# Kernel optimization log

Measured on AMD Instinct MI355X. Metric: run time of the kernel, lower is better.

## Reference

```python
import jax, jax.numpy as jnp
import numpy as np

H = 1024
F = 1024


def _lstm_cell(x, h, c, Wih, Whh, b):
    # PyTorch gate order: i, f, g, o
    gates = x @ Wih.T + h @ Whh.T + b
    i, f, g, o = jnp.split(gates, 4, axis=-1)
    c = jax.nn.sigmoid(f) * c + jax.nn.sigmoid(i) * jnp.tanh(g)
    h = jax.nn.sigmoid(o) * jnp.tanh(c)
    return h, c


def setup_inputs() -> dict:
    key = jax.random.key(0)
    ks = iter(jax.random.split(key, 32))
    def rn(shape, s=0.05):
        return (s * jax.random.normal(next(ks), shape)).astype(jnp.float32)
    return {
        "tsn_feat_seq": rn((4096, F), 1.0),
        "W_fe": rn((H, F)), "b_fe": rn((H,)),
        "gW_ih0": rn((4 * H, 2 * H)), "gW_ihR": rn((4, 4 * H, H)),
        "gW_hh": rn((5, 4 * H, H)), "gb_ih": rn((5, 4 * H)), "gb_hh": rn((5, 4 * H)),
        "rW_ih": rn((4 * H, 2 * H)), "rW_hh": rn((4 * H, H)),
        "rb_ih": rn((4 * H,)), "rb_hh": rn((4 * H,)),
        "Wp": rn((H, 3 * H)), "bp": rn((H,)),
        "We2a": rn((2513, H)), "be2a": rn((2513,)),
        "We2v": rn((125, H)), "be2v": rn((125,)),
        "We2n": rn((352, H)), "be2n": rn((352,)),
    }


def reference(tsn_feat_seq, W_fe, b_fe, gW_ih0, gW_ihR, gW_hh, gb_ih, gb_hh,
              rW_ih, rW_hh, rb_ih, rb_hh, Wp, bp,
              We2a, be2a, We2v, be2v, We2n, be2n):
    # feat embedding of max-pooled TSN features (batch is always 1 after max)
    fs = jnp.max(tsn_feat_seq, axis=0) @ W_fe.T + b_fe          # [H]
    cur_action = (fs @ We2a.T + be2a)[None, :]                   # [1, 2513]

    # 5-layer goal LSTM, single time step, zero initial states;
    # input = concat(feat_state, zero action_state)
    z = jnp.zeros(H, fs.dtype)
    x = jnp.concatenate([fs, z])                                 # [2H]
    h, _ = _lstm_cell(x, z, z, gW_ih0, gW_hh[0], gb_ih[0] + gb_hh[0])
    for k in range(4):
        h, _ = _lstm_cell(h, z, z, gW_ihR[k], gW_hh[k + 1], gb_ih[k + 1] + gb_hh[k + 1])
    g = h                                                        # goal_state [H]

    rb = rb_ih + rb_hh

    def expand(a_in, f_in, best_d, best_f):
        # 10 single-layer LSTM steps with FIXED input (as in the source loop)
        xin = jnp.concatenate([a_in, f_in])                      # [2H]
        def rnn_step(carry, _):
            hh, cc = carry
            hh, cc = _lstm_cell(xin, hh, cc, rW_ih, rW_hh, rb)
            return (hh, cc), hh
        _, a_js = jax.lax.scan(rnn_step, (z, z), None, length=10)   # [10, H]
        # featpredictor: relu(Linear(concat(feat, action, goal))); dropout = eval identity
        pf = jnp.concatenate([jnp.broadcast_to(f_in, (10, H)), a_js,
                              jnp.broadcast_to(g, (10, H))], axis=1)  # [10, 3H]
        nfs = jax.nn.relu(pf @ Wp.T + bp)                        # [10, H]
        # sequential greedy best-feat update defines the scores (order matters)
        def score_step(carry, nf):
            bd, bf = carry
            d = jnp.sum((nf - g) ** 2) / H
            s = bd - d
            upd = d < bd
            return (jnp.where(upd, d, bd), jnp.where(upd, nf, bf)), s
        (bd, bf), scores = jax.lax.scan(score_step, (best_d, best_f), nfs)
        return a_js, nfs, scores, bd, bf

    # expansion 1: root node (action=0, feat=fs); best_feat_state starts at fs
    bd0 = jnp.sum((fs - g) ** 2) / H
    a1, f1, s1, bd1, bf1 = expand(z, fs, bd0, fs)
    # priority queue pops lowest score -> expansion 2 from that node
    i_star = jnp.argmin(s1)
    a2in = a1[i_star]
    f2in = f1[i_star]
    a2, f2, s2, _, _ = expand(a2in, f2in, bd1, bf1)

    # chain means: exp1 chain = [root, child]; exp2 chain = [root, n2, child]
    am = jnp.concatenate([a1 / 2.0, (a2in + a2) / 3.0], axis=0)        # [20, H]
    fm = jnp.concatenate([(fs + f1) / 2.0, (fs + f2in + f2) / 3.0], axis=0)
    scores = jnp.concatenate([s1.at[i_star].set(jnp.inf), s2])          # popped node removed
    _, idx = jax.lax.top_k(-scores, 2)                                  # 2 lowest scores, ascending
    pa = am[idx]                                                        # [2, H]
    pfeat = fm[idx]                                                     # [2, H]
    pgoal = jnp.broadcast_to(g, (2, H))

    pred_actions = pa @ We2a.T + be2a                                   # [2, 2513]
    pred_verbs = pa @ We2v.T + be2v                                     # [2, 125]
    pred_nouns = pa @ We2n.T + be2n                                     # [2, 352]
    # returned feat_state is the feat of the last popped (expanded) node
    return (pred_actions, pred_verbs, pred_nouns, pfeat, pgoal, f2in[None, :], cur_action)
```

## Files before the change

kernel.cpp:

```cpp
#include <hip/hip_runtime.h>
#include <math.h>


__device__ __forceinline__ float sigf(float x) { return 1.0f / (1.0f + expf(-x)); }

__device__ __forceinline__ float wave_red(float v) {
#pragma unroll
    for (int s = 32; s; s >>= 1) v += __shfl_down(v, s, 64);
    return v;
}

__device__ __forceinline__ float dotf(const float* __restrict__ w,
                                      const float* __restrict__ x, int lane) {
    float acc = 0.f;
#pragma unroll
    for (int j = 0; j < 4; ++j) {
        float4 a = *reinterpret_cast<const float4*>(w + j * 256 + lane * 4);
        float4 b = *reinterpret_cast<const float4*>(x + j * 256 + lane * 4);
        acc += a.x * b.x + a.y * b.y + a.z * b.z + a.w * b.w;
    }
    return acc;
}

__global__ void colmax_part_k(const float* __restrict__ tsn, float* __restrict__ part) {
    int tid = threadIdx.x;
    const float4* t4 = reinterpret_cast<const float4*>(tsn);
    float4 m = make_float4(-INFINITY, -INFINITY, -INFINITY, -INFINITY);
    int r0 = blockIdx.x * 512;
    for (int r = r0; r < r0 + 512; ++r) {
        float4 v = t4[(size_t)r * 256 + tid];
        m.x = fmaxf(m.x, v.x); m.y = fmaxf(m.y, v.y);
        m.z = fmaxf(m.z, v.z); m.w = fmaxf(m.w, v.w);
    }
    reinterpret_cast<float4*>(part + (size_t)blockIdx.x * 1024)[tid] = m;
}
__global__ void colmax_fin_k(const float* __restrict__ part, float* __restrict__ maxv) {
    int c = blockIdx.x * 256 + threadIdx.x;
    float m = -INFINITY;
    for (int b = 0; b < 8; ++b) m = fmaxf(m, part[b * 1024 + c]);
    maxv[c] = m;
}

__global__ void gemv_k(const float* __restrict__ W, int ld, int nrows,
                       const float* __restrict__ xA, int offA,
                       const float* __restrict__ xB, int offB,
                       const float* __restrict__ b1,
                       const float* __restrict__ b2,
                       float* __restrict__ yF, float* __restrict__ yOut) {
    int wave = threadIdx.x >> 6, lane = threadIdx.x & 63;
    int row = blockIdx.x * 4 + wave;
    if (row >= nrows) return;
    const float* wr = W + (size_t)row * ld;
    float acc = 0.f;
    if (xA) acc += dotf(wr + offA, xA, lane);
    if (xB) acc += dotf(wr + offB, xB, lane);
    acc = wave_red(acc);
    if (lane == 0) {
        if (b1) acc += b1[row];
        if (b2) acc += b2[row];
        if (yF) yF[row] = acc;
        if (yOut) yOut[row] = acc;
    }
}

__global__ void lstm_fused_k(const float* __restrict__ W, int ld, int off,
                             const float* __restrict__ x,
                             const float* __restrict__ b1,
                             const float* __restrict__ b2,
                             const float* __restrict__ gx,
                             const float* __restrict__ cc_in,
                             float* __restrict__ cc_out,
                             float* __restrict__ h_out) {
    __shared__ float glds[4][4];
    int wave = threadIdx.x >> 6, lane = threadIdx.x & 63;
    int j0 = blockIdx.x * 4;
#pragma unroll
    for (int jj = 0; jj < 4; ++jj) {
        int row = wave * 1024 + j0 + jj;
        float acc = dotf(W + (size_t)row * ld + off, x, lane);
        acc = wave_red(acc);
        if (lane == 0) {
            if (b1) acc += b1[row];
            if (b2) acc += b2[row];
            if (gx) acc += gx[row];
            glds[wave][jj] = acc;
        }
    }
    __syncthreads();
    if (threadIdx.x < 4) {
        int jj = threadIdx.x, j = j0 + jj;
        float gi = glds[0][jj], gf = glds[1][jj], gg = glds[2][jj], go = glds[3][jj];
        float c = sigf(gi) * tanhf(gg);
        if (cc_in) c += sigf(gf) * cc_in[j];
        float h = sigf(go) * tanhf(c);
        if (cc_out) cc_out[j] = c;
        h_out[j] = h;
    }
}

__global__ void cell0_k(const float* __restrict__ gx, float* __restrict__ cc_out,
                        float* __restrict__ h_out) {
    int j = blockIdx.x * 256 + threadIdx.x;
    float gi = gx[j], gg = gx[2048 + j], go = gx[3072 + j];
    float c = sigf(gi) * tanhf(gg);
    float h = sigf(go) * tanhf(c);
    cc_out[j] = c;
    h_out[j] = h;
}

__global__ void nfs_k(const float* __restrict__ Wp, const float* __restrict__ ajs,
                      const float* __restrict__ sv, float* __restrict__ nfs) {
    int wave = threadIdx.x >> 6, lane = threadIdx.x & 63;
    int i = blockIdx.x * 4 + wave;
    const float* wr = Wp + (size_t)i * 3072 + 1024;
    float wf[16];
#pragma unroll
    for (int j = 0; j < 4; ++j) {
        float4 a = *reinterpret_cast<const float4*>(wr + j * 256 + lane * 4);
        wf[j * 4 + 0] = a.x; wf[j * 4 + 1] = a.y; wf[j * 4 + 2] = a.z; wf[j * 4 + 3] = a.w;
    }
    float acc[10];
#pragma unroll
    for (int t = 0; t < 10; ++t) acc[t] = 0.f;
#pragma unroll
    for (int t = 0; t < 10; ++t) {
        const float* a = ajs + t * 1024;
#pragma unroll
        for (int j = 0; j < 4; ++j) {
            float4 b = *reinterpret_cast<const float4*>(a + j * 256 + lane * 4);
            acc[t] += wf[j * 4 + 0] * b.x + wf[j * 4 + 1] * b.y +
                      wf[j * 4 + 2] * b.z + wf[j * 4 + 3] * b.w;
        }
    }
#pragma unroll
    for (int t = 0; t < 10; ++t) {
        float r = wave_red(acc[t]);
        if (lane == 0) nfs[t * 1024 + i] = fmaxf(sv[i] + r, 0.f);
    }
}

__global__ void scores1_k(const float* __restrict__ nfs1, const float* __restrict__ g,
                          const float* __restrict__ fs, const float* __restrict__ ajs1,
                          float* __restrict__ s1, float* __restrict__ bd1_out,
                          int* __restrict__ istar_out, float* __restrict__ a2in,
                          float* __restrict__ f2in, float* __restrict__ out_f2in) {
    __shared__ float red[256];
    __shared__ float d[11];
    __shared__ int istar_sh;
    int tid = threadIdx.x;
    for (int t = 0; t < 11; ++t) {
        const float* v = (t < 10) ? (nfs1 + t * 1024) : fs;
        float p = 0.f;
        for (int j = tid * 4; j < tid * 4 + 4; ++j) { float df = v[j] - g[j]; p += df * df; }
        red[tid] = p; __syncthreads();
        for (int s = 128; s; s >>= 1) { if (tid < s) red[tid] += red[tid + s]; __syncthreads(); }
        if (tid == 0) d[t] = red[0] * (1.0f / 1024.0f);
        __syncthreads();
    }
    if (tid == 0) {
        float bd = d[10];
        float smin = INFINITY; int im = 0;
        for (int t = 0; t < 10; ++t) {
            float s = bd - d[t];
            s1[t] = s;
            if (s < smin) { smin = s; im = t; }
            if (d[t] < bd) bd = d[t];
        }
        *bd1_out = bd; *istar_out = im; istar_sh = im;
    }
    __syncthreads();
    int im = istar_sh;
    for (int j = tid; j < 1024; j += 256) {
        float a = ajs1[im * 1024 + j], f = nfs1[im * 1024 + j];
        a2in[j] = a; f2in[j] = f; out_f2in[j] = f;
    }
}

__global__ void scores2_k(const float* __restrict__ nfs2, const float* __restrict__ g,
                          const float* __restrict__ fs, const float* __restrict__ ajs1,
                          const float* __restrict__ nfs1, const float* __restrict__ ajs2,
                          const float* __restrict__ a2in, const float* __restrict__ f2in,
                          const float* __restrict__ s1, const float* __restrict__ bd1,
                          const int* __restrict__ istar, float* __restrict__ pa,
                          float* __restrict__ out) {
    __shared__ float red[256];
    __shared__ float d[10];
    __shared__ int sel[2];
    int tid = threadIdx.x;
    for (int t = 0; t < 10; ++t) {
        const float* v = nfs2 + t * 1024;
        float p = 0.f;
        for (int j = tid * 4; j < tid * 4 + 4; ++j) { float df = v[j] - g[j]; p += df * df; }
        red[tid] = p; __syncthreads();
        for (int s = 128; s; s >>= 1) { if (tid < s) red[tid] += red[tid + s]; __syncthreads(); }
        if (tid == 0) d[t] = red[0] * (1.0f / 1024.0f);
        __syncthreads();
    }
    if (tid == 0) {
        float sc[20];
        int im = *istar;
        for (int t = 0; t < 10; ++t) sc[t] = (t == im) ? INFINITY : s1[t];
        float bd = *bd1;
        for (int t = 0; t < 10; ++t) {
            float s = bd - d[t];
            sc[10 + t] = s;
            if (d[t] < bd) bd = d[t];
        }
        int i0 = 0; float m0 = INFINITY;
        for (int t = 0; t < 20; ++t) if (sc[t] < m0) { m0 = sc[t]; i0 = t; }
        int i1 = 0; float m1 = INFINITY;
        for (int t = 0; t < 20; ++t) { if (t == i0) continue; if (sc[t] < m1) { m1 = sc[t]; i1 = t; } }
        sel[0] = i0; sel[1] = i1;
    }
    __syncthreads();
    for (int p = 0; p < 2; ++p) {
        int idx = sel[p];
        for (int j = tid; j < 1024; j += 256) {
            float av, fv;
            if (idx < 10) {
                av = ajs1[idx * 1024 + j] * 0.5f;
                fv = (fs[j] + nfs1[idx * 1024 + j]) * 0.5f;
            } else {
                int t = idx - 10;
                av = (a2in[j] + ajs2[t * 1024 + j]) * (1.0f / 3.0f);
                fv = (fs[j] + f2in[j] + nfs2[t * 1024 + j]) * (1.0f / 3.0f);
            }
            pa[p * 1024 + j] = av;
            out[5980 + p * 1024 + j] = fv;
            out[8028 + p * 1024 + j] = g[j];
        }
    }
}

__global__ void heads_k(const float* __restrict__ We2a, const float* __restrict__ be2a,
                        const float* __restrict__ We2v, const float* __restrict__ be2v,
                        const float* __restrict__ We2n, const float* __restrict__ be2n,
                        const float* __restrict__ pa, float* __restrict__ out) {
    int wave = threadIdx.x >> 6, lane = threadIdx.x & 63;
    int task = blockIdx.x * 4 + wave;
    if (task >= 5980) return;
    int p = (task < 2990) ? 0 : 1;
    int r = task - p * 2990;
    const float* W; const float* b; int outoff, rr;
    if (r < 2513)      { W = We2a; b = be2a; rr = r;        outoff = p * 2513 + rr; }
    else if (r < 2638) { W = We2v; b = be2v; rr = r - 2513; outoff = 5026 + p * 125 + rr; }
    else               { W = We2n; b = be2n; rr = r - 2638; outoff = 5276 + p * 352 + rr; }
    float acc = dotf(W + (size_t)rr * 1024, pa + p * 1024, lane);
    acc = wave_red(acc);
    if (lane == 0) out[outoff] = acc + b[rr];
}

extern "C" void kernel_launch(void* const* d_in, const int* in_sizes, int n_in,
                              void* d_out, int out_size, void* d_ws, size_t ws_size,
                              hipStream_t stream) {
    const float* tsn    = (const float*)d_in[0];
    const float* W_fe   = (const float*)d_in[1];
    const float* b_fe   = (const float*)d_in[2];
    const float* gW_ih0 = (const float*)d_in[3];
    const float* gW_ihR = (const float*)d_in[4];
    const float* gb_ih  = (const float*)d_in[6];
    const float* gb_hh  = (const float*)d_in[7];
    const float* rW_ih  = (const float*)d_in[8];
    const float* rW_hh  = (const float*)d_in[9];
    const float* rb_ih  = (const float*)d_in[10];
    const float* rb_hh  = (const float*)d_in[11];
    const float* Wp     = (const float*)d_in[12];
    const float* bp     = (const float*)d_in[13];
    const float* We2a   = (const float*)d_in[14];
    const float* be2a   = (const float*)d_in[15];
    const float* We2v   = (const float*)d_in[16];
    const float* be2v   = (const float*)d_in[17];
    const float* We2n   = (const float*)d_in[18];
    const float* be2n   = (const float*)d_in[19];
    float* out = (float*)d_out;

    float* w = (float*)d_ws;
    float* part  = w + 0;
    float* maxv  = w + 8192;
    float* fs    = w + 9216;
    float* hgA   = w + 10240;
    float* hgB   = w + 11264;
    float* gx    = w + 12288;
    float* ajs1  = w + 16384;
    float* nfs1  = w + 26624;
    float* ajs2  = w + 36864;
    float* nfs2  = w + 47104;
    float* cc0   = w + 57344;
    float* cc1   = w + 58368;
    float* sv    = w + 59392;
    float* a2in  = w + 60416;
    float* f2in  = w + 61440;
    float* pa    = w + 62464;
    float* s1    = w + 64512;
    float* bd1   = w + 64524;
    int*   istar = (int*)(w + 64528);

    colmax_part_k<<<8, 256, 0, stream>>>(tsn, part);
    colmax_fin_k<<<4, 256, 0, stream>>>(part, maxv);
    gemv_k<<<256, 256, 0, stream>>>(W_fe, 1024, 1024, maxv, 0, nullptr, 0, b_fe, nullptr, fs, nullptr);
    gemv_k<<<629, 256, 0, stream>>>(We2a, 1024, 2513, fs, 0, nullptr, 0, be2a, nullptr, nullptr, out + 11100);

    lstm_fused_k<<<256, 256, 0, stream>>>(gW_ih0, 2048, 0, fs, gb_ih, gb_hh, nullptr, nullptr, nullptr, hgA);
    lstm_fused_k<<<256, 256, 0, stream>>>(gW_ihR + (size_t)0 * 4194304, 1024, 0, hgA, gb_ih + 1 * 4096, gb_hh + 1 * 4096, nullptr, nullptr, nullptr, hgB);
    lstm_fused_k<<<256, 256, 0, stream>>>(gW_ihR + (size_t)1 * 4194304, 1024, 0, hgB, gb_ih + 2 * 4096, gb_hh + 2 * 4096, nullptr, nullptr, nullptr, hgA);
    lstm_fused_k<<<256, 256, 0, stream>>>(gW_ihR + (size_t)2 * 4194304, 1024, 0, hgA, gb_ih + 3 * 4096, gb_hh + 3 * 4096, nullptr, nullptr, nullptr, hgB);
    lstm_fused_k<<<256, 256, 0, stream>>>(gW_ihR + (size_t)3 * 4194304, 1024, 0, hgB, gb_ih + 4 * 4096, gb_hh + 4 * 4096, nullptr, nullptr, nullptr, hgA);
    float* g = hgA;

    gemv_k<<<1024, 256, 0, stream>>>(rW_ih, 2048, 4096, nullptr, 0, fs, 1024, rb_ih, rb_hh, gx, nullptr);
    cell0_k<<<4, 256, 0, stream>>>(gx, cc0, ajs1);
    for (int t = 1; t < 10; ++t) {
        float* cin = ((t - 1) & 1) ? cc1 : cc0;
        float* cout = (t & 1) ? cc1 : cc0;
        lstm_fused_k<<<256, 256, 0, stream>>>(rW_hh, 1024, 0, ajs1 + (t - 1) * 1024,
                                              nullptr, nullptr, gx, cin, cout, ajs1 + t * 1024);
    }
    gemv_k<<<256, 256, 0, stream>>>(Wp, 3072, 1024, fs, 0, g, 2048, bp, nullptr, sv, nullptr);
    nfs_k<<<256, 256, 0, stream>>>(Wp, ajs1, sv, nfs1);
    scores1_k<<<1, 256, 0, stream>>>(nfs1, g, fs, ajs1, s1, bd1, istar, a2in, f2in, out + 10076);

    gemv_k<<<1024, 256, 0, stream>>>(rW_ih, 2048, 4096, a2in, 0, f2in, 1024, rb_ih, rb_hh, gx, nullptr);
    cell0_k<<<4, 256, 0, stream>>>(gx, cc0, ajs2);
    for (int t = 1; t < 10; ++t) {
        float* cin = ((t - 1) & 1) ? cc1 : cc0;
        float* cout = (t & 1) ? cc1 : cc0;
        lstm_fused_k<<<256, 256, 0, stream>>>(rW_hh, 1024, 0, ajs2 + (t - 1) * 1024,
                                              nullptr, nullptr, gx, cin, cout, ajs2 + t * 1024);
    }
    gemv_k<<<256, 256, 0, stream>>>(Wp, 3072, 1024, f2in, 0, g, 2048, bp, nullptr, sv, nullptr);
    nfs_k<<<256, 256, 0, stream>>>(Wp, ajs2, sv, nfs2);
    scores2_k<<<1, 256, 0, stream>>>(nfs2, g, fs, ajs1, nfs1, ajs2, a2in, f2in, s1, bd1, istar, pa, out);

    heads_k<<<1495, 256, 0, stream>>>(We2a, be2a, We2v, be2v, We2n, be2n, pa, out);
}
```

Baseline: 499.7 us.

## Widen LSTM/GEMV blocks, atomic column max, fuse gx+cell0, defer cur_action head

The two-kernel column max is replaced by 256 blocks doing atomicMax on order-preserving encoded floats, and the max decode is fused into the W_fe GEMV. LSTM step kernels move to 512-thread blocks with 8 waves, each handling two gate rows, and the input-gate GEMV is fused with the first cell update. The nfs kernel spreads its timesteps over 8 waves, and the cur_action head GEMV is folded into the final heads launch. Together these cut launch count and raise parallelism for the latency-bound sequence of small kernels, at the cost of atomics and an extra init launch.

Result: faster. 420.9 us (-15.8%).

```diff
diff --git a/kernel.cpp b/kernel.cpp
--- a/kernel.cpp
+++ b/kernel.cpp
@@ -8,6 +8,14 @@
 #pragma unroll
     for (int s = 32; s; s >>= 1) v += __shfl_down(v, s, 64);
     return v;
+}
+
+__device__ __forceinline__ unsigned encf(float f) {
+    unsigned u = __float_as_uint(f);
+    return (u & 0x80000000u) ? ~u : (u | 0x80000000u);
+}
+__device__ __forceinline__ float decf(unsigned e) {
+    return (e & 0x80000000u) ? __uint_as_float(e ^ 0x80000000u) : __uint_as_float(~e);
 }
 
 __device__ __forceinline__ float dotf(const float* __restrict__ w,
@@ -22,33 +30,48 @@
     return acc;
 }
 
-__global__ void colmax_part_k(const float* __restrict__ tsn, float* __restrict__ part) {
+__global__ void init_k(unsigned* u) { u[blockIdx.x * 256 + threadIdx.x] = 0; }
+
+__global__ void colmax_k(const float* __restrict__ tsn, unsigned* __restrict__ maxenc) {
     int tid = threadIdx.x;
     const float4* t4 = reinterpret_cast<const float4*>(tsn);
     float4 m = make_float4(-INFINITY, -INFINITY, -INFINITY, -INFINITY);
-    int r0 = blockIdx.x * 512;
-    for (int r = r0; r < r0 + 512; ++r) {
+    int r0 = blockIdx.x * 16;
+    for (int r = r0; r < r0 + 16; ++r) {
         float4 v = t4[(size_t)r * 256 + tid];
         m.x = fmaxf(m.x, v.x); m.y = fmaxf(m.y, v.y);
         m.z = fmaxf(m.z, v.z); m.w = fmaxf(m.w, v.w);
     }
-    reinterpret_cast<float4*>(part + (size_t)blockIdx.x * 1024)[tid] = m;
-}
-__global__ void colmax_fin_k(const float* __restrict__ part, float* __restrict__ maxv) {
-    int c = blockIdx.x * 256 + threadIdx.x;
-    float m = -INFINITY;
-    for (int b = 0; b < 8; ++b) m = fmaxf(m, part[b * 1024 + c]);
-    maxv[c] = m;
+    atomicMax(&maxenc[4 * tid + 0], encf(m.x));
+    atomicMax(&maxenc[4 * tid + 1], encf(m.y));
+    atomicMax(&maxenc[4 * tid + 2], encf(m.z));
+    atomicMax(&maxenc[4 * tid + 3], encf(m.w));
+}
+
+__global__ void fsdec_k(const float* __restrict__ W_fe, const unsigned* __restrict__ maxenc,
+                        const float* __restrict__ b_fe, float* __restrict__ fs) {
+    int w = threadIdx.x >> 6, lane = threadIdx.x & 63;
+    int row = blockIdx.x * 4 + w;
+    const float* wr = W_fe + (size_t)row * 1024;
+    const uint4* e4 = reinterpret_cast<const uint4*>(maxenc);
+    float acc = 0.f;
+#pragma unroll
+    for (int k = 0; k < 4; ++k) {
+        float4 a = *reinterpret_cast<const float4*>(wr + k * 256 + lane * 4);
+        uint4 e = e4[k * 64 + lane];
+        acc += a.x * decf(e.x) + a.y * decf(e.y) + a.z * decf(e.z) + a.w * decf(e.w);
+    }
+    acc = wave_red(acc);
+    if (lane == 0) fs[row] = acc + b_fe[row];
 }
 
 __global__ void gemv_k(const float* __restrict__ W, int ld, int nrows,
                        const float* __restrict__ xA, int offA,
                        const float* __restrict__ xB, int offB,
-                       const float* __restrict__ b1,
-                       const float* __restrict__ b2,
-                       float* __restrict__ yF, float* __restrict__ yOut) {
-    int wave = threadIdx.x >> 6, lane = threadIdx.x & 63;
-    int row = blockIdx.x * 4 + wave;
+                       const float* __restrict__ b1, const float* __restrict__ b2,
+                       float* __restrict__ y) {
+    int w = threadIdx.x >> 6, lane = threadIdx.x & 63;
+    int row = blockIdx.x * 4 + w;
     if (row >= nrows) return;
     const float* wr = W + (size_t)row * ld;
     float acc = 0.f;
@@ -58,38 +81,37 @@
     if (lane == 0) {
         if (b1) acc += b1[row];
         if (b2) acc += b2[row];
-        if (yF) yF[row] = acc;
-        if (yOut) yOut[row] = acc;
-    }
-}
-
-__global__ void lstm_fused_k(const float* __restrict__ W, int ld, int off,
-                             const float* __restrict__ x,
-                             const float* __restrict__ b1,
-                             const float* __restrict__ b2,
-                             const float* __restrict__ gx,
-                             const float* __restrict__ cc_in,
-                             float* __restrict__ cc_out,
-                             float* __restrict__ h_out) {
+        y[row] = acc;
+    }
+}
+
+__global__ void lstm8_k(const float* __restrict__ W, int ld, int off,
+                        const float* __restrict__ x,
+                        const float* __restrict__ b1, const float* __restrict__ b2,
+                        const float* __restrict__ gx,
+                        const float* __restrict__ cc_in,
+                        float* __restrict__ cc_out, float* __restrict__ h_out) {
     __shared__ float glds[4][4];
-    int wave = threadIdx.x >> 6, lane = threadIdx.x & 63;
-    int j0 = blockIdx.x * 4;
-#pragma unroll
-    for (int jj = 0; jj < 4; ++jj) {
-        int row = wave * 1024 + j0 + jj;
-        float acc = dotf(W + (size_t)row * ld + off, x, lane);
-        acc = wave_red(acc);
-        if (lane == 0) {
-            if (b1) acc += b1[row];
-            if (b2) acc += b2[row];
-            if (gx) acc += gx[row];
-            glds[wave][jj] = acc;
-        }
+    int tid = threadIdx.x, w = tid >> 6, lane = tid & 63;
+    int gate = w >> 1, jp = (w & 1) * 2, j0 = blockIdx.x * 4;
+    int r0 = (gate << 10) + j0 + jp;
+    const float* wr0 = W + (size_t)r0 * ld + off;
+    const float* wr1 = wr0 + ld;
+    float a0 = dotf(wr0, x, lane);
+    float a1 = dotf(wr1, x, lane);
+    a0 = wave_red(a0);
+    a1 = wave_red(a1);
+    if (lane == 0) {
+        if (b1) { a0 += b1[r0]; a1 += b1[r0 + 1]; }
+        if (b2) { a0 += b2[r0]; a1 += b2[r0 + 1]; }
+        if (gx) { a0 += gx[r0]; a1 += gx[r0 + 1]; }
+        glds[gate][jp] = a0;
+        glds[gate][jp + 1] = a1;
     }
     __syncthreads();
-    if (threadIdx.x < 4) {
-        int jj = threadIdx.x, j = j0 + jj;
-        float gi = glds[0][jj], gf = glds[1][jj], gg = glds[2][jj], go = glds[3][jj];
+    if (tid < 4) {
+        int j = j0 + tid;
+        float gi = glds[0][tid], gf = glds[1][tid], gg = glds[2][tid], go = glds[3][tid];
         float c = sigf(gi) * tanhf(gg);
         if (cc_in) c += sigf(gf) * cc_in[j];
         float h = sigf(go) * tanhf(c);
@@ -98,44 +120,67 @@
     }
 }
 
-__global__ void cell0_k(const float* __restrict__ gx, float* __restrict__ cc_out,
-                        float* __restrict__ h_out) {
-    int j = blockIdx.x * 256 + threadIdx.x;
-    float gi = gx[j], gg = gx[2048 + j], go = gx[3072 + j];
-    float c = sigf(gi) * tanhf(gg);
-    float h = sigf(go) * tanhf(c);
-    cc_out[j] = c;
-    h_out[j] = h;
-}
-
-__global__ void nfs_k(const float* __restrict__ Wp, const float* __restrict__ ajs,
-                      const float* __restrict__ sv, float* __restrict__ nfs) {
-    int wave = threadIdx.x >> 6, lane = threadIdx.x & 63;
-    int i = blockIdx.x * 4 + wave;
+__global__ void gxcell_k(const float* __restrict__ W, int ld,
+                         const float* __restrict__ xA, int offA,
+                         const float* __restrict__ xB, int offB,
+                         const float* __restrict__ b1, const float* __restrict__ b2,
+                         float* __restrict__ gx, float* __restrict__ cc_out,
+                         float* __restrict__ h_out) {
+    __shared__ float glds[4][4];
+    int tid = threadIdx.x, w = tid >> 6, lane = tid & 63;
+    int gate = w >> 1, jp = (w & 1) * 2, j0 = blockIdx.x * 4;
+    int r0 = (gate << 10) + j0 + jp;
+    const float* wr0 = W + (size_t)r0 * ld;
+    const float* wr1 = wr0 + ld;
+    float a0 = 0.f, a1 = 0.f;
+    if (xA) { a0 += dotf(wr0 + offA, xA, lane); a1 += dotf(wr1 + offA, xA, lane); }
+    if (xB) { a0 += dotf(wr0 + offB, xB, lane); a1 += dotf(wr1 + offB, xB, lane); }
+    a0 = wave_red(a0);
+    a1 = wave_red(a1);
+    if (lane == 0) {
+        a0 += b1[r0]; a1 += b1[r0 + 1];
+        a0 += b2[r0]; a1 += b2[r0 + 1];
+        gx[r0] = a0;
+        gx[r0 + 1] = a1;
+        glds[gate][jp] = a0;
+        glds[gate][jp + 1] = a1;
+    }
+    __syncthreads();
+    if (tid < 4) {
+        int j = j0 + tid;
+        float gi = glds[0][tid], gg = glds[2][tid], go = glds[3][tid];
+        float c = sigf(gi) * tanhf(gg);
+        float h = sigf(go) * tanhf(c);
+        cc_out[j] = c;
+        h_out[j] = h;
+    }
+}
+
+__global__ void nfs8_k(const float* __restrict__ Wp, const float* __restrict__ ajs,
+                       const float* __restrict__ sv, float* __restrict__ nfs) {
+    int tid = threadIdx.x, w = tid >> 6, lane = tid & 63;
+    int i = blockIdx.x * 4 + (w & 3);
+    int tp = w >> 2;
     const float* wr = Wp + (size_t)i * 3072 + 1024;
     float wf[16];
 #pragma unroll
-    for (int j = 0; j < 4; ++j) {
-        float4 a = *reinterpret_cast<const float4*>(wr + j * 256 + lane * 4);
-        wf[j * 4 + 0] = a.x; wf[j * 4 + 1] = a.y; wf[j * 4 + 2] = a.z; wf[j * 4 + 3] = a.w;
-    }
-    float acc[10];
-#pragma unroll
-    for (int t = 0; t < 10; ++t) acc[t] = 0.f;
-#pragma unroll
-    for (int t = 0; t < 10; ++t) {
-        const float* a = ajs + t * 1024;
-#pragma unroll
-        for (int j = 0; j < 4; ++j) {
-            float4 b = *reinterpret_cast<const float4*>(a + j * 256 + lane * 4);
-            acc[t] += wf[j * 4 + 0] * b.x + wf[j * 4 + 1] * b.y +
-                      wf[j * 4 + 2] * b.z + wf[j * 4 + 3] * b.w;
+    for (int k = 0; k < 4; ++k) {
+        float4 a = *reinterpret_cast<const float4*>(wr + k * 256 + lane * 4);
+        wf[4 * k] = a.x; wf[4 * k + 1] = a.y; wf[4 * k + 2] = a.z; wf[4 * k + 3] = a.w;
+    }
+#pragma unroll 1
+    for (int ii = 0; ii < 5; ++ii) {
+        int t = tp + 2 * ii;
+        const float* av = ajs + t * 1024;
+        float acc = 0.f;
+#pragma unroll
+        for (int k = 0; k < 4; ++k) {
+            float4 v = *reinterpret_cast<const float4*>(av + k * 256 + lane * 4);
+            acc += wf[4 * k] * v.x + wf[4 * k + 1] * v.y + wf[4 * k + 2] * v.z +
+                   wf[4 * k + 3] * v.w;
         }
-    }
-#pragma unroll
-    for (int t = 0; t < 10; ++t) {
-        float r = wave_red(acc[t]);
-        if (lane == 0) nfs[t * 1024 + i] = fmaxf(sv[i] + r, 0.f);
+        acc = wave_red(acc);
+        if (lane == 0) nfs[t * 1024 + i] = fmaxf(sv[i] + acc, 0.f);
     }
 }
 
@@ -235,19 +280,27 @@
 __global__ void heads_k(const float* __restrict__ We2a, const float* __restrict__ be2a,
                         const float* __restrict__ We2v, const float* __restrict__ be2v,
                         const float* __restrict__ We2n, const float* __restrict__ be2n,
-                        const float* __restrict__ pa, float* __restrict__ out) {
-    int wave = threadIdx.x >> 6, lane = threadIdx.x & 63;
-    int task = blockIdx.x * 4 + wave;
-    if (task >= 5980) return;
-    int p = (task < 2990) ? 0 : 1;
-    int r = task - p * 2990;
-    const float* W; const float* b; int outoff, rr;
-    if (r < 2513)      { W = We2a; b = be2a; rr = r;        outoff = p * 2513 + rr; }
-    else if (r < 2638) { W = We2v; b = be2v; rr = r - 2513; outoff = 5026 + p * 125 + rr; }
-    else               { W = We2n; b = be2n; rr = r - 2638; outoff = 5276 + p * 352 + rr; }
-    float acc = dotf(W + (size_t)rr * 1024, pa + p * 1024, lane);
-    acc = wave_red(acc);
-    if (lane == 0) out[outoff] = acc + b[rr];
+                        const float* __restrict__ pa, const float* __restrict__ fs,
+                        float* __restrict__ out) {
+    int w = threadIdx.x >> 6, lane = threadIdx.x & 63;
+    int task = blockIdx.x * 8 + w;
+    if (task >= 8493) return;
+    if (task < 5980) {
+        int p = (task < 2990) ? 0 : 1;
+        int r = task - p * 2990;
+        const float* W; const float* b; int rr, outoff;
+        if (r < 2513)      { W = We2a; b = be2a; rr = r;        outoff = p * 2513 + rr; }
+        else if (r < 2638) { W = We2v; b = be2v; rr = r - 2513; outoff = 5026 + p * 125 + rr; }
+        else               { W = We2n; b = be2n; rr = r - 2638; outoff = 5276 + p * 352 + rr; }
+        float acc = dotf(W + (size_t)rr * 1024, pa + p * 1024, lane);
+        acc = wave_red(acc);
+        if (lane == 0) out[outoff] = acc + b[rr];
+    } else {
+        int r = task - 5980;
+        float acc = dotf(We2a + (size_t)r * 1024, fs, lane);
+        acc = wave_red(acc);
+        if (lane == 0) out[11100 + r] = acc + be2a[r];
+    }
 }
 
 extern "C" void kernel_launch(void* const* d_in, const int* in_sizes, int n_in,
@@ -275,61 +328,65 @@
     float* out = (float*)d_out;
 
     float* w = (float*)d_ws;
-    float* part  = w + 0;
-    float* maxv  = w + 8192;
-    float* fs    = w + 9216;
-    float* hgA   = w + 10240;
-    float* hgB   = w + 11264;
-    float* gx    = w + 12288;
-    float* ajs1  = w + 16384;
-    float* nfs1  = w + 26624;
-    float* ajs2  = w + 36864;
-    float* nfs2  = w + 47104;
-    float* cc0   = w + 57344;
-    float* cc1   = w + 58368;
-    float* sv    = w + 59392;
-    float* a2in  = w + 60416;
-    float* f2in  = w + 61440;
-    float* pa    = w + 62464;
-    float* s1    = w + 64512;
-    float* bd1   = w + 64524;
-    int*   istar = (int*)(w + 64528);
-
-    colmax_part_k<<<8, 256, 0, stream>>>(tsn, part);
-    colmax_fin_k<<<4, 256, 0, stream>>>(part, maxv);
-    gemv_k<<<256, 256, 0, stream>>>(W_fe, 1024, 1024, maxv, 0, nullptr, 0, b_fe, nullptr, fs, nullptr);
-    gemv_k<<<629, 256, 0, stream>>>(We2a, 1024, 2513, fs, 0, nullptr, 0, be2a, nullptr, nullptr, out + 11100);
-
-    lstm_fused_k<<<256, 256, 0, stream>>>(gW_ih0, 2048, 0, fs, gb_ih, gb_hh, nullptr, nullptr, nullptr, hgA);
-    lstm_fused_k<<<256, 256, 0, stream>>>(gW_ihR + (size_t)0 * 4194304, 1024, 0, hgA, gb_ih + 1 * 4096, gb_hh + 1 * 4096, nullptr, nullptr, nullptr, hgB);
-    lstm_fused_k<<<256, 256, 0, stream>>>(gW_ihR + (size_t)1 * 4194304, 1024, 0, hgB, gb_ih + 2 * 4096, gb_hh + 2 * 4096, nullptr, nullptr, nullptr, hgA);
-    lstm_fused_k<<<256, 256, 0, stream>>>(gW_ihR + (size_t)2 * 4194304, 1024, 0, hgA, gb_ih + 3 * 4096, gb_hh + 3 * 4096, nullptr, nullptr, nullptr, hgB);
-    lstm_fused_k<<<256, 256, 0, stream>>>(gW_ihR + (size_t)3 * 4194304, 1024, 0, hgB, gb_ih + 4 * 4096, gb_hh + 4 * 4096, nullptr, nullptr, nullptr, hgA);
+    unsigned* maxenc = (unsigned*)d_ws;
+    float* fs    = w + 1024;
+    float* hgA   = w + 2048;
+    float* hgB   = w + 3072;
+    float* gx    = w + 4096;
+    float* cc0   = w + 8192;
+    float* cc1   = w + 9216;
+    float* sv    = w + 10240;
+    float* a2in  = w + 11264;
+    float* f2in  = w + 12288;
+    float* pa    = w + 13312;
+    float* ajs1  = w + 15360;
+    float* nfs1  = w + 25600;
+    float* ajs2  = w + 35840;
+    float* nfs2  = w + 46080;
+    float* s1    = w + 56320;
+    float* bd1   = w + 56332;
+    int*   istar = (int*)(w + 56336);
+
+    init_k<<<4, 256, 0, stream>>>(maxenc);
+    colmax_k<<<256, 256, 0, stream>>>(tsn, maxenc);
+    fsdec_k<<<256, 256, 0, stream>>>(W_fe, maxenc, b_fe, fs);
+
+    lstm8_k<<<256, 512, 0, stream>>>(gW_ih0, 2048, 0, fs, gb_ih, gb_hh,
+                                     nullptr, nullptr, nullptr, hgA);
+    lstm8_k<<<256, 512, 0, stream>>>(gW_ihR + (size_t)0 * 4194304, 1024, 0, hgA,
+                                     gb_ih + 4096, gb_hh + 4096, nullptr, nullptr, nullptr, hgB);
+    lstm8_k<<<256, 512, 0, stream>>>(gW_ihR + (size_t)1 * 4194304, 1024, 0, hgB,
+                                     gb_ih + 8192, gb_hh + 8192, nullptr, nullptr, nullptr, hgA);
+    lstm8_k<<<256, 512, 0, stream>>>(gW_ihR + (size_t)2 * 4194304, 1024, 0, hgA,
+                                     gb_ih + 12288, gb_hh + 12288, nullptr, nullptr, nullptr, hgB);
+    lstm8_k<<<256, 512, 0, stream>>>(gW_ihR + (size_t)3 * 4194304, 1024, 0, hgB,
+                                     gb_ih + 16384, gb_hh + 16384, nullptr, nullptr, nullptr, hgA);
     float* g = hgA;
 
-    gemv_k<<<1024, 256, 0, stream>>>(rW_ih, 2048, 4096, nullptr, 0, fs, 1024, rb_ih, rb_hh, gx, nullptr);
-    cell0_k<<<4, 256, 0, stream>>>(gx, cc0, ajs1);
+    gxcell_k<<<256, 512, 0, stream>>>(rW_ih, 2048, nullptr, 0, fs, 1024,
+                                      rb_ih, rb_hh, gx, cc0, ajs1);
     for (int t = 1; t < 10; ++t) {
         float* cin = ((t - 1) & 1) ? cc1 : cc0;
         float* cout = (t & 1) ? cc1 : cc0;
-        lstm_fused_k<<<256, 256, 0, stream>>>(rW_hh, 1024, 0, ajs1 + (t - 1) * 1024,
-                                              nullptr, nullptr, gx, cin, cout, ajs1 + t * 1024);
-    }
-    gemv_k<<<256, 256, 0, stream>>>(Wp, 3072, 1024, fs, 0, g, 2048, bp, nullptr, sv, nullptr);
-    nfs_k<<<256, 256, 0, stream>>>(Wp, ajs1, sv, nfs1);
+        lstm8_k<<<256, 512, 0, stream>>>(rW_hh, 1024, 0, ajs1 + (t - 1) * 1024,
+                                         nullptr, nullptr, gx, cin, cout, ajs1 + t * 1024);
+    }
+    gemv_k<<<256, 256, 0, stream>>>(Wp, 3072, 1024, fs, 0, g, 2048, bp, nullptr, sv);
+    nfs8_k<<<256, 512, 0, stream>>>(Wp, ajs1, sv, nfs1);
     scores1_k<<<1, 256, 0, stream>>>(nfs1, g, fs, ajs1, s1, bd1, istar, a2in, f2in, out + 10076);
 
-    gemv_k<<<1024, 256, 0, stream>>>(rW_ih, 2048, 4096, a2in, 0, f2in, 1024, rb_ih, rb_hh, gx, nullptr);
-    cell0_k<<<4, 256, 0, stream>>>(gx, cc0, ajs2);
+    gxcell_k<<<256, 512, 0, stream>>>(rW_ih, 2048, a2in, 0, f2in, 1024,
+                                      rb_ih, rb_hh, gx, cc0, ajs2);
     for (int t = 1; t < 10; ++t) {
         float* cin = ((t - 1) & 1) ? cc1 : cc0;
         float* cout = (t & 1) ? cc1 : cc0;
-        lstm_fused_k<<<256, 256, 0, stream>>>(rW_hh, 1024, 0, ajs2 + (t - 1) * 1024,
-                                              nullptr, nullptr, gx, cin, cout, ajs2 + t * 1024);
-    }
-    gemv_k<<<256, 256, 0, stream>>>(Wp, 3072, 1024, f2in, 0, g, 2048, bp, nullptr, sv, nullptr);
-    nfs_k<<<256, 256, 0, stream>>>(Wp, ajs2, sv, nfs2);
-    scores2_k<<<1, 256, 0, stream>>>(nfs2, g, fs, ajs1, nfs1, ajs2, a2in, f2in, s1, bd1, istar, pa, out);
-
-    heads_k<<<1495, 256, 0, stream>>>(We2a, be2a, We2v, be2v, We2n, be2n, pa, out);
-}
+        lstm8_k<<<256, 512, 0, stream>>>(rW_hh, 1024, 0, ajs2 + (t - 1) * 1024,
+                                         nullptr, nullptr, gx, cin, cout, ajs2 + t * 1024);
+    }
+    gemv_k<<<256, 256, 0, stream>>>(Wp, 3072, 1024, f2in, 0, g, 2048, bp, nullptr, sv);
+    nfs8_k<<<256, 512, 0, stream>>>(Wp, ajs2, sv, nfs2);
+    scores2_k<<<1, 256, 0, stream>>>(nfs2, g, fs, ajs1, nfs1, ajs2, a2in, f2in,
+                                     s1, bd1, istar, pa, out);
+
+    heads_k<<<1062, 512, 0, stream>>>(We2a, be2a, We2v, be2v, We2n, be2n, pa, fs, out);
+}
```
